# Optimization experiments

Hardware: AMD Instinct MI355X
Metric: run time of the kernel (lower is better)

The kernel has to match this reference:

```python
import jax, jax.numpy as jnp
import numpy as np


def setup_inputs() -> dict:
    key = jax.random.key(0)
    k1, k2, k3, k4 = jax.random.split(key, 4)
    B, T, C = 4, 2048, 1024
    x = jax.random.normal(k1, (B, T, C), dtype=jnp.float32)
    scale = 1.0 / np.sqrt(C)
    Wq = jax.random.normal(k2, (C, C), dtype=jnp.float32) * scale
    Wk = jax.random.normal(k3, (C, C), dtype=jnp.float32) * scale
    Wv = jax.random.normal(k4, (C, C), dtype=jnp.float32) * scale
    return {"x": x, "Wq": Wq, "Wk": Wk, "Wv": Wv}


def reference(x, Wq, Wk, Wv):
    # x: [B, T, C]; torch Linear(no bias): y = x @ W.T
    B, T, C = x.shape
    q = jnp.einsum('btc,dc->btd', x, Wq)
    k = jnp.einsum('btc,dc->btd', x, Wk)
    v = jnp.einsum('btc,dc->btd', x, Wv)
    scale = jnp.asarray(C, x.dtype) ** -0.5
    qk = jnp.einsum('bqd,bkd->bqk', q, k) * scale  # [B, T, T]
    causal = jnp.tril(jnp.ones((T, T), dtype=bool))
    qk = jnp.where(causal, qk, -jnp.inf)
    attn = jax.nn.softmax(qk, axis=-1)
    out = jnp.einsum('bqk,bkd->bqd', attn, v)
    return out
```

## Files before the change

kernel.cpp:

```cpp
#include <hip/hip_runtime.h>

typedef __attribute__((ext_vector_type(8))) short  short8;
typedef __attribute__((ext_vector_type(4))) short  short4v;
typedef __attribute__((ext_vector_type(4))) float  floatx4;

__device__ inline short f2bf(float f) {
    union { float f; unsigned u; } v; v.f = f;
    unsigned r = v.u + 0x7fffu + ((v.u >> 16) & 1u);
    return (short)(r >> 16);
}

typedef const __attribute__((address_space(1))) unsigned int* gp1_t;
typedef __attribute__((address_space(3))) unsigned int* lp3_t;

__device__ __attribute__((always_inline)) inline void gl_lds16(const short* g, short* l) {
    __builtin_amdgcn_global_load_lds((gp1_t)g, (lp3_t)l, 16, 0, 0);
}

__device__ __attribute__((always_inline)) inline void gemm_bt_core(
    const short* __restrict__ Ag, const short* __restrict__ Bg,
    int lda, int ldb, int kmax,
    short* As, short* Bs, floatx4 acc[4][4])
{
    const int t    = threadIdx.x;
    const int srow = t >> 3;
    const int scol = (t & 7) * 8;
    const int lane = t & 63;
    const int wid  = t >> 6;
    const int wx   = wid & 1, wy = wid >> 1;
    const int lm   = lane & 15, lq = lane >> 4;

    for (int k0 = 0; k0 < kmax; k0 += 64) {
        __syncthreads();
#pragma unroll
        for (int i = 0; i < 4; ++i) {
            gl_lds16(Ag + (size_t)(i * 32 + srow) * lda + k0 + scol,
                     As + (i * 32 + srow) * 64 + scol);
            gl_lds16(Bg + (size_t)(i * 32 + srow) * ldb + k0 + scol,
                     Bs + (i * 32 + srow) * 64 + scol);
        }
        __syncthreads();

#pragma unroll
        for (int ks = 0; ks < 2; ++ks) {
            short8 af[4], bfr[4];
#pragma unroll
            for (int mi = 0; mi < 4; ++mi)
                af[mi] = *(const short8*)(As + (wy * 64 + mi * 16 + lm) * 64 + ks * 32 + lq * 8);
#pragma unroll
            for (int ni = 0; ni < 4; ++ni)
                bfr[ni] = *(const short8*)(Bs + (wx * 64 + ni * 16 + lm) * 64 + ks * 32 + lq * 8);
#pragma unroll
            for (int mi = 0; mi < 4; ++mi)
#pragma unroll
                for (int ni = 0; ni < 4; ++ni)
                    acc[mi][ni] = __builtin_amdgcn_mfma_f32_16x16x32_bf16(
                        af[mi], bfr[ni], acc[mi][ni], 0, 0, 0);
        }
    }
}

__global__ void cast_all(const float* __restrict__ x,
                         const float* __restrict__ Wq,
                         const float* __restrict__ Wk,
                         const float* __restrict__ Wv,
                         short* __restrict__ xb, short* __restrict__ wb)
{
    size_t v = (size_t)blockIdx.x * 256 + threadIdx.x;
    const float* src; short* dst; size_t off;
    if (v < 2097152)      { src = x;  dst = xb;           off = v; }
    else if (v < 2359296) { src = Wq; dst = wb;           off = v - 2097152; }
    else if (v < 2621440) { src = Wk; dst = wb + 1048576; off = v - 2359296; }
    else if (v < 2883584) { src = Wv; dst = wb + 2097152; off = v - 2621440; }
    else return;
    floatx4 vv = ((const floatx4*)src)[off];
    short4v s;
#pragma unroll
    for (int e = 0; e < 4; ++e) s[e] = f2bf(vv[e]);
    ((short4v*)dst)[off] = s;
}

__global__ __launch_bounds__(256, 4) void qkv_gemm(
    const short* __restrict__ xb, const short* __restrict__ wb,
    short* __restrict__ qb, short* __restrict__ kb, short* __restrict__ vt)
{
    __shared__ short As[128 * 64];
    __shared__ short Bs[128 * 64];

    const int m0    = blockIdx.x * 128;
    const int which = blockIdx.y >> 3;
    const int n0    = (blockIdx.y & 7) * 128;

    floatx4 acc[4][4];
    floatx4 zero = {0.f, 0.f, 0.f, 0.f};
#pragma unroll
    for (int i = 0; i < 4; ++i)
#pragma unroll
        for (int j = 0; j < 4; ++j) acc[i][j] = zero;

    gemm_bt_core(xb + (size_t)m0 * 1024,
                 wb + (size_t)blockIdx.y * 128 * 1024,
                 1024, 1024, 1024, As, Bs, acc);

    const int lane = threadIdx.x & 63, wid = threadIdx.x >> 6;
    const int wx = wid & 1, wy = wid >> 1, lm = lane & 15, lq = lane >> 4;
#pragma unroll
    for (int mi = 0; mi < 4; ++mi)
#pragma unroll
        for (int ni = 0; ni < 4; ++ni)
#pragma unroll
            for (int r = 0; r < 4; ++r) {
                int row = m0 + wy * 64 + mi * 16 + lq * 4 + r;
                int col = n0 + wx * 64 + ni * 16 + lm;
                short bvv = f2bf(acc[mi][ni][r]);
                if (which == 2) {
                    int bb = row >> 11, tt = row & 2047;
                    vt[((size_t)bb * 1024 + col) * 2048 + tt] = bvv;
                } else if (which == 1) {
                    kb[(size_t)row * 1024 + col] = bvv;
                } else {
                    qb[(size_t)row * 1024 + col] = bvv;
                }
            }
}

__global__ __launch_bounds__(256, 4) void sqk_gemm(
    const short* __restrict__ qb, const short* __restrict__ kb,
    short* __restrict__ P)
{
    int idx = blockIdx.x;
    int i = 0;
    while ((i + 1) * (i + 2) / 2 <= idx) ++i;
    const int j = idx - i * (i + 1) / 2;
    const int b = blockIdx.y;

    __shared__ short As[128 * 64];
    __shared__ short Bs[128 * 64];

    floatx4 acc[4][4];
    floatx4 zero = {0.f, 0.f, 0.f, 0.f};
#pragma unroll
    for (int a = 0; a < 4; ++a)
#pragma unroll
        for (int c = 0; c < 4; ++c) acc[a][c] = zero;

    gemm_bt_core(qb + ((size_t)(b * 2048 + i * 128)) * 1024,
                 kb + ((size_t)(b * 2048 + j * 128)) * 1024,
                 1024, 1024, 1024, As, Bs, acc);

    const float sscl = 0.03125f * 1.44269504089f;
    const bool  diag = (i == j);
    const int lane = threadIdx.x & 63, wid = threadIdx.x >> 6;
    const int wx = wid & 1, wy = wid >> 1, lm = lane & 15, lq = lane >> 4;

#pragma unroll
    for (int mi = 0; mi < 4; ++mi)
#pragma unroll
        for (int r = 0; r < 4; ++r) {
            const int lrow = wy * 64 + mi * 16 + lq * 4 + r;
            const int grow = i * 128 + lrow;
            short* prow = P + ((size_t)b * 2048 + grow) * 2048 + j * 128;
#pragma unroll
            for (int ni = 0; ni < 4; ++ni) {
                const int lcol = wx * 64 + ni * 16 + lm;
                float p = exp2f(acc[mi][ni][r] * sscl);
                if (diag && lcol > lrow) p = 0.f;
                prow[lcol] = f2bf(p);
            }
        }
}

__global__ __launch_bounds__(256, 3) void pv_gemm(
    const short* __restrict__ P, const short* __restrict__ vt,
    float* __restrict__ out)
{
    const int x = blockIdx.x, i = blockIdx.y, b = blockIdx.z;
    const int n0 = x * 128;
    const int kmax = (i + 1) * 128;

    __shared__ short As[128 * 64];
    __shared__ short Bs[128 * 64];

    const int t    = threadIdx.x;
    const int srow = t >> 3;
    const int scol = (t & 7) * 8;
    const int lane = t & 63;
    const int wid  = t >> 6;
    const int wx   = wid & 1, wy = wid >> 1;
    const int lm   = lane & 15, lq = lane >> 4;

    const short* Ag = P  + ((size_t)b * 2048 + i * 128) * 2048;
    const short* Bg = vt + ((size_t)b * 1024 + n0) * 2048;

    floatx4 acc[4][5];
    floatx4 zero = {0.f, 0.f, 0.f, 0.f};
#pragma unroll
    for (int a = 0; a < 4; ++a)
#pragma unroll
        for (int c = 0; c < 5; ++c) acc[a][c] = zero;

    short8 vones;
#pragma unroll
    for (int e = 0; e < 8; ++e) vones[e] = (short)0x3F80;

    for (int k0 = 0; k0 < kmax; k0 += 64) {
        __syncthreads();
#pragma unroll
        for (int q = 0; q < 4; ++q) {
            gl_lds16(Ag + (size_t)(q * 32 + srow) * 2048 + k0 + scol,
                     As + (q * 32 + srow) * 64 + scol);
            gl_lds16(Bg + (size_t)(q * 32 + srow) * 2048 + k0 + scol,
                     Bs + (q * 32 + srow) * 64 + scol);
        }
        __syncthreads();

#pragma unroll
        for (int ks = 0; ks < 2; ++ks) {
            short8 af[4], bfr[4];
#pragma unroll
            for (int mi = 0; mi < 4; ++mi)
                af[mi] = *(const short8*)(As + (wy * 64 + mi * 16 + lm) * 64 + ks * 32 + lq * 8);
#pragma unroll
            for (int ni = 0; ni < 4; ++ni)
                bfr[ni] = *(const short8*)(Bs + (wx * 64 + ni * 16 + lm) * 64 + ks * 32 + lq * 8);
#pragma unroll
            for (int mi = 0; mi < 4; ++mi) {
#pragma unroll
                for (int ni = 0; ni < 4; ++ni)
                    acc[mi][ni] = __builtin_amdgcn_mfma_f32_16x16x32_bf16(
                        af[mi], bfr[ni], acc[mi][ni], 0, 0, 0);
                acc[mi][4] = __builtin_amdgcn_mfma_f32_16x16x32_bf16(
                    af[mi], vones, acc[mi][4], 0, 0, 0);
            }
        }
    }

#pragma unroll
    for (int mi = 0; mi < 4; ++mi)
#pragma unroll
        for (int r = 0; r < 4; ++r) {
            const int grow = b * 2048 + i * 128 + wy * 64 + mi * 16 + lq * 4 + r;
            const float li = 1.0f / acc[mi][4][r];
#pragma unroll
            for (int ni = 0; ni < 4; ++ni)
                out[(size_t)grow * 1024 + n0 + wx * 64 + ni * 16 + lm] =
                    acc[mi][ni][r] * li;
        }
}

extern "C" void kernel_launch(void* const* d_in, const int* in_sizes, int n_in,
                              void* d_out, int out_size, void* d_ws, size_t ws_size,
                              hipStream_t stream)
{
    (void)in_sizes; (void)n_in; (void)out_size; (void)ws_size;
    const float* x  = (const float*)d_in[0];
    const float* Wq = (const float*)d_in[1];
    const float* Wk = (const float*)d_in[2];
    const float* Wv = (const float*)d_in[3];
    float* out = (float*)d_out;

    char* base = (char*)d_ws;
    short* xb = (short*)(base);
    short* wb = (short*)(base + 16777216);
    short* qb = (short*)(base + 23068672);
    short* kb = (short*)(base + 39845888);
    short* vt = (short*)(base + 56623104);
    short* P  = (short*)(base + 73400320);

    cast_all<<<11264, 256, 0, stream>>>(x, Wq, Wk, Wv, xb, wb);
    qkv_gemm<<<dim3(64, 24), 256, 0, stream>>>(xb, wb, qb, kb, vt);
    sqk_gemm<<<dim3(136, 4), 256, 0, stream>>>(qb, kb, P);
    pv_gemm<<<dim3(8, 16, 4), 256, 0, stream>>>(P, vt, out);
}
```

Baseline: 251.2 us.

## Double-buffer LDS tiles in score and PV GEMMs, schedule longest PV rows first

Adds a double-buffered GEMM core that prefetches the next K-slice into a second LDS buffer while MFMAs consume the current one. This needs only one barrier per iteration instead of two. The core is used in the QK^T score kernel and the P·V kernel; the P·V kernel folds in its row-sum ones-column accumulation. P·V blocks are also reordered so the longest causal rows launch first, and launch bounds are lowered because the LDS footprint doubles. The cost is lower occupancy per CU in exchange for hiding global-to-LDS load latency.

```diff
diff --git a/kernel.cpp b/kernel.cpp
--- a/kernel.cpp
+++ b/kernel.cpp
@@ -56,6 +56,71 @@
                 for (int ni = 0; ni < 4; ++ni)
                     acc[mi][ni] = __builtin_amdgcn_mfma_f32_16x16x32_bf16(
                         af[mi], bfr[ni], acc[mi][ni], 0, 0, 0);
+        }
+    }
+}
+
+template <bool SUMCOL>
+__device__ __attribute__((always_inline)) inline void gemm_bt_dbuf(
+    const short* __restrict__ Ag, const short* __restrict__ Bg,
+    int lda, int ldb, int kmax,
+    short* As, short* Bs, floatx4 acc[4][4], floatx4 accl[4])
+{
+    const int t    = threadIdx.x;
+    const int srow = t >> 3;
+    const int scol = (t & 7) * 8;
+    const int lane = t & 63;
+    const int wid  = t >> 6;
+    const int wx   = wid & 1, wy = wid >> 1;
+    const int lm   = lane & 15, lq = lane >> 4;
+
+    short8 vones;
+#pragma unroll
+    for (int e = 0; e < 8; ++e) vones[e] = (short)0x3F80;
+
+#pragma unroll
+    for (int i = 0; i < 4; ++i) {
+        gl_lds16(Ag + (size_t)(i * 32 + srow) * lda + scol, As + (i * 32 + srow) * 64 + scol);
+        gl_lds16(Bg + (size_t)(i * 32 + srow) * ldb + scol, Bs + (i * 32 + srow) * 64 + scol);
+    }
+
+    const int nit = kmax >> 6;
+    for (int it = 0; it < nit; ++it) {
+        const int p = it & 1;
+        short* Ac = As + p * (128 * 64);
+        short* Bc = Bs + p * (128 * 64);
+        __syncthreads();
+        if (it + 1 < nit) {
+            const int k0 = (it + 1) << 6;
+            short* An = As + (p ^ 1) * (128 * 64);
+            short* Bn = Bs + (p ^ 1) * (128 * 64);
+#pragma unroll
+            for (int i = 0; i < 4; ++i) {
+                gl_lds16(Ag + (size_t)(i * 32 + srow) * lda + k0 + scol,
+                         An + (i * 32 + srow) * 64 + scol);
+                gl_lds16(Bg + (size_t)(i * 32 + srow) * ldb + k0 + scol,
+                         Bn + (i * 32 + srow) * 64 + scol);
+            }
+        }
+#pragma unroll
+        for (int ks = 0; ks < 2; ++ks) {
+            short8 af[4], bfr[4];
+#pragma unroll
+            for (int mi = 0; mi < 4; ++mi)
+                af[mi] = *(const short8*)(Ac + (wy * 64 + mi * 16 + lm) * 64 + ks * 32 + lq * 8);
+#pragma unroll
+            for (int ni = 0; ni < 4; ++ni)
+                bfr[ni] = *(const short8*)(Bc + (wx * 64 + ni * 16 + lm) * 64 + ks * 32 + lq * 8);
+#pragma unroll
+            for (int mi = 0; mi < 4; ++mi) {
+#pragma unroll
+                for (int ni = 0; ni < 4; ++ni)
+                    acc[mi][ni] = __builtin_amdgcn_mfma_f32_16x16x32_bf16(
+                        af[mi], bfr[ni], acc[mi][ni], 0, 0, 0);
+                if (SUMCOL)
+                    accl[mi] = __builtin_amdgcn_mfma_f32_16x16x32_bf16(
+                        af[mi], vones, accl[mi], 0, 0, 0);
+            }
         }
     }
 }
@@ -80,7 +145,7 @@
     ((short4v*)dst)[off] = s;
 }
 
-__global__ __launch_bounds__(256, 4) void qkv_gemm(
+__global__ __launch_bounds__(256, 3) void qkv_gemm(
     const short* __restrict__ xb, const short* __restrict__ wb,
     short* __restrict__ qb, short* __restrict__ kb, short* __restrict__ vt)
 {
@@ -124,7 +189,7 @@
             }
 }
 
-__global__ __launch_bounds__(256, 4) void sqk_gemm(
+__global__ __launch_bounds__(256, 2) void sqk_gemm(
     const short* __restrict__ qb, const short* __restrict__ kb,
     short* __restrict__ P)
 {
@@ -134,19 +199,22 @@
     const int j = idx - i * (i + 1) / 2;
     const int b = blockIdx.y;
 
-    __shared__ short As[128 * 64];
-    __shared__ short Bs[128 * 64];
+    __shared__ short As[2 * 128 * 64];
+    __shared__ short Bs[2 * 128 * 64];
 
     floatx4 acc[4][4];
+    floatx4 dummy[4];
     floatx4 zero = {0.f, 0.f, 0.f, 0.f};
 #pragma unroll
-    for (int a = 0; a < 4; ++a)
+    for (int a = 0; a < 4; ++a) {
+        dummy[a] = zero;
 #pragma unroll
         for (int c = 0; c < 4; ++c) acc[a][c] = zero;
-
-    gemm_bt_core(qb + ((size_t)(b * 2048 + i * 128)) * 1024,
-                 kb + ((size_t)(b * 2048 + j * 128)) * 1024,
-                 1024, 1024, 1024, As, Bs, acc);
+    }
+
+    gemm_bt_dbuf<false>(qb + ((size_t)(b * 2048 + i * 128)) * 1024,
+                        kb + ((size_t)(b * 2048 + j * 128)) * 1024,
+                        1024, 1024, 1024, As, Bs, acc, dummy);
 
     const float sscl = 0.03125f * 1.44269504089f;
     const bool  diag = (i == j);
@@ -170,77 +238,39 @@
         }
 }
 
-__global__ __launch_bounds__(256, 3) void pv_gemm(
+__global__ __launch_bounds__(256, 2) void pv_gemm(
     const short* __restrict__ P, const short* __restrict__ vt,
     float* __restrict__ out)
 {
-    const int x = blockIdx.x, i = blockIdx.y, b = blockIdx.z;
+    const int x = blockIdx.x, i = 15 - blockIdx.y, b = blockIdx.z;
     const int n0 = x * 128;
     const int kmax = (i + 1) * 128;
 
-    __shared__ short As[128 * 64];
-    __shared__ short Bs[128 * 64];
-
-    const int t    = threadIdx.x;
-    const int srow = t >> 3;
-    const int scol = (t & 7) * 8;
-    const int lane = t & 63;
-    const int wid  = t >> 6;
-    const int wx   = wid & 1, wy = wid >> 1;
-    const int lm   = lane & 15, lq = lane >> 4;
-
-    const short* Ag = P  + ((size_t)b * 2048 + i * 128) * 2048;
-    const short* Bg = vt + ((size_t)b * 1024 + n0) * 2048;
-
-    floatx4 acc[4][5];
+    __shared__ short As[2 * 128 * 64];
+    __shared__ short Bs[2 * 128 * 64];
+
+    floatx4 acc[4][4];
+    floatx4 accl[4];
     floatx4 zero = {0.f, 0.f, 0.f, 0.f};
 #pragma unroll
-    for (int a = 0; a < 4; ++a)
-#pragma unroll
-        for (int c = 0; c < 5; ++c) acc[a][c] = zero;
-
-    short8 vones;
-#pragma unroll
-    for (int e = 0; e < 8; ++e) vones[e] = (short)0x3F80;
-
-    for (int k0 = 0; k0 < kmax; k0 += 64) {
-        __syncthreads();
-#pragma unroll
-        for (int q = 0; q < 4; ++q) {
-            gl_lds16(Ag + (size_t)(q * 32 + srow) * 2048 + k0 + scol,
-                     As + (q * 32 + srow) * 64 + scol);
-            gl_lds16(Bg + (size_t)(q * 32 + srow) * 2048 + k0 + scol,
-                     Bs + (q * 32 + srow) * 64 + scol);
-        }
-        __syncthreads();
-
-#pragma unroll
-        for (int ks = 0; ks < 2; ++ks) {
-            short8 af[4], bfr[4];
-#pragma unroll
-            for (int mi = 0; mi < 4; ++mi)
-                af[mi] = *(const short8*)(As + (wy * 64 + mi * 16 + lm) * 64 + ks * 32 + lq * 8);
-#pragma unroll
-            for (int ni = 0; ni < 4; ++ni)
-                bfr[ni] = *(const short8*)(Bs + (wx * 64 + ni * 16 + lm) * 64 + ks * 32 + lq * 8);
-#pragma unroll
-            for (int mi = 0; mi < 4; ++mi) {
-#pragma unroll
-                for (int ni = 0; ni < 4; ++ni)
-                    acc[mi][ni] = __builtin_amdgcn_mfma_f32_16x16x32_bf16(
-                        af[mi], bfr[ni], acc[mi][ni], 0, 0, 0);
-                acc[mi][4] = __builtin_amdgcn_mfma_f32_16x16x32_bf16(
-                    af[mi], vones, acc[mi][4], 0, 0, 0);
-            }
-        }
-    }
-
+    for (int a = 0; a < 4; ++a) {
+        accl[a] = zero;
+#pragma unroll
+        for (int c = 0; c < 4; ++c) acc[a][c] = zero;
+    }
+
+    gemm_bt_dbuf<true>(P  + ((size_t)b * 2048 + i * 128) * 2048,
+                       vt + ((size_t)b * 1024 + n0) * 2048,
+                       2048, 2048, kmax, As, Bs, acc, accl);
+
+    const int lane = threadIdx.x & 63, wid = threadIdx.x >> 6;
+    const int wx = wid & 1, wy = wid >> 1, lm = lane & 15, lq = lane >> 4;
 #pragma unroll
     for (int mi = 0; mi < 4; ++mi)
 #pragma unroll
         for (int r = 0; r < 4; ++r) {
             const int grow = b * 2048 + i * 128 + wy * 64 + mi * 16 + lq * 4 + r;
-            const float li = 1.0f / acc[mi][4][r];
+            const float li = 1.0f / accl[mi][r];
 #pragma unroll
             for (int ni = 0; ni < 4; ++ni)
                 out[(size_t)grow * 1024 + n0 + wx * 64 + ni * 16 + lm] =
```

Result: slower. 268.2 us (+6.8%).
